# Performance work log

Measured on AMD Instinct MI355X. Metric: run time of the kernel, lower is better.

The kernel has to match this reference:

```python
import jax, jax.numpy as jnp
import numpy as np

GH, GW = 16, 16          # group_size
DIM = 512
H = 8                    # num_heads
PD = DIM // 16           # pos_dim = (dim//4)//4 = 32
B = 256                  # number of groups (batch*windows)
N = GH * GW


def _make_bias_tables():
    # biases buffer: all 2D relative offsets, shape [(2GH-1)*(2GW-1), 2]
    h = np.arange(1 - GH, GH)
    w = np.arange(1 - GW, GW)
    bh, bw = np.meshgrid(h, w, indexing='ij')
    biases = np.stack([bh, bw]).reshape(2, -1).T.astype(np.float32)
    # relative_position_index: [N, N] lookup into the bias table
    ch, cw = np.meshgrid(np.arange(GH), np.arange(GW), indexing='ij')
    coords = np.stack([ch, cw]).reshape(2, -1)            # [2, N]
    rel = coords[:, :, None] - coords[:, None, :]         # [2, N, N]
    rel = rel.transpose(1, 2, 0).copy()                   # [N, N, 2]
    rel[:, :, 0] += GH - 1
    rel[:, :, 1] += GW - 1
    rel[:, :, 0] *= 2 * GW - 1
    idx = rel.sum(-1)
    return biases, idx.astype(np.int32)


def _ln(x, g, b, eps=1e-5):
    m = x.mean(-1, keepdims=True)
    v = ((x - m) ** 2).mean(-1, keepdims=True)
    return (x - m) / jnp.sqrt(v + eps) * g + b


def setup_inputs() -> dict:
    key = jax.random.key(0)
    ks = jax.random.split(key, 16)
    s = 0.02
    biases_np, idx_np = _make_bias_tables()
    return {
        'x': jax.random.normal(ks[0], (B, N, DIM), dtype=jnp.float32),
        'qkv_w': jax.random.normal(ks[1], (DIM, 3 * DIM), dtype=jnp.float32) * s,
        'qkv_b': jnp.zeros((3 * DIM,), jnp.float32),
        'proj_w': jax.random.normal(ks[2], (DIM, DIM), dtype=jnp.float32) * s,
        'proj_b': jnp.zeros((DIM,), jnp.float32),
        'p1_w': jax.random.normal(ks[3], (2, PD), dtype=jnp.float32) * s,
        'p1_b': jnp.zeros((PD,), jnp.float32),
        'g1': jnp.ones((PD,), jnp.float32), 'b1': jnp.zeros((PD,), jnp.float32),
        'p2_w': jax.random.normal(ks[4], (PD, PD), dtype=jnp.float32) * s,
        'p2_b': jnp.zeros((PD,), jnp.float32),
        'g2': jnp.ones((PD,), jnp.float32), 'b2': jnp.zeros((PD,), jnp.float32),
        'p3_w': jax.random.normal(ks[5], (PD, PD), dtype=jnp.float32) * s,
        'p3_b': jnp.zeros((PD,), jnp.float32),
        'g3': jnp.ones((PD,), jnp.float32), 'b3': jnp.zeros((PD,), jnp.float32),
        'p4_w': jax.random.normal(ks[6], (PD, H), dtype=jnp.float32) * s,
        'p4_b': jnp.zeros((H,), jnp.float32),
        'biases': jnp.asarray(biases_np),
        'rel_idx': jnp.asarray(idx_np),
    }


def reference(x, qkv_w, qkv_b, proj_w, proj_b,
              p1_w, p1_b, g1, b1, p2_w, p2_b, g2, b2,
              p3_w, p3_b, g3, b3, p4_w, p4_b, biases, rel_idx):
    Bn, Nn, C = x.shape
    hd = C // H
    scale = hd ** -0.5
    qkv = (x @ qkv_w + qkv_b).reshape(Bn, Nn, 3, H, hd).transpose(2, 0, 3, 1, 4)
    q, k, v = qkv[0] * scale, qkv[1], qkv[2]      # [B, H, N, hd]
    attn = jnp.einsum('bhnd,bhmd->bhnm', q, k)    # [B, H, N, N]
    # dynamic position bias MLP on the offset table
    h1 = jax.nn.relu(_ln(biases @ p1_w + p1_b, g1, b1))
    h2 = jax.nn.relu(_ln(h1 @ p2_w + p2_b, g2, b2))
    h3 = jax.nn.relu(_ln(h2 @ p3_w + p3_b, g3, b3))
    pos = h3 @ p4_w + p4_b                        # [L, H]
    rpb = pos[rel_idx.reshape(-1)].reshape(Nn, Nn, H).transpose(2, 0, 1)  # [H, N, N]
    attn = jax.nn.softmax(attn + rpb[None], axis=-1)
    out = jnp.einsum('bhnm,bhmd->bhnd', attn, v)
    out = out.transpose(0, 2, 1, 3).reshape(Bn, Nn, C)
    return out @ proj_w + proj_b
```

## Files before the change

kernel.cpp:

```cpp
#include <hip/hip_runtime.h>
#include <stdint.h>

typedef __bf16 bf16x8 __attribute__((ext_vector_type(8)));
typedef float  f32x4  __attribute__((ext_vector_type(4)));
typedef unsigned short ushort_t;

#define MFMA16(a,b,c) __builtin_amdgcn_mfma_f32_16x16x32_bf16((a),(b),(c),0,0,0)

#define GLOAD16(gsrc, ldst) \
    __builtin_amdgcn_global_load_lds((const __attribute__((address_space(1))) void*)(gsrc), \
                                     (__attribute__((address_space(3))) void*)(ldst), 16, 0, 0)

#define BATCH 256
#define NTOK  256
#define DIM   512
#define NH    8
#define HD    64
#define PD    32
#define LTAB  961
#define LOG2E 1.4426950408889634f

#define POS_OFF   0
#define RPB_OFF   32768
#define WQKV_OFF  (RPB_OFF + 2097152)
#define WPROJ_OFF (WQKV_OFF + 1572864)
#define QKV_OFF   (WPROJ_OFF + 524288)
#define AOUT_OFF  (QKV_OFF + 201326592)
#define XB_OFF    AOUT_OFF

__device__ __forceinline__ ushort_t f2bf(float f) {
    unsigned int u = __builtin_bit_cast(unsigned int, f);
    u += 0x7FFFu + ((u >> 16) & 1u);
    return (ushort_t)(u >> 16);
}
__device__ __forceinline__ ushort_t cvt_bf16(float f) {
    __bf16 h = (__bf16)f;
    return __builtin_bit_cast(ushort_t, h);
}
__device__ __forceinline__ float exp2_raw(float x) {
    float r;
    asm("v_exp_f32 %0, %1" : "=v"(r) : "v"(x));
    return r;
}

#define PRO_CONV  16384
#define PRO_TQKV  (PRO_CONV + 192)
#define PRO_TPROJ (PRO_TQKV + 64)
#define PRO_TOTAL (PRO_TPROJ + 121)

__device__ __forceinline__ void transpose_body(
    const float* __restrict__ src, ushort_t* __restrict__ dst,
    int K, int Nn, int bid, int t, ushort_t (*tile)[65])
{
    int tiles_n = Nn >> 6;
    int tn = bid % tiles_n, tk = bid / tiles_n;
    int n0 = tn * 64, k0 = tk * 64;
#pragma unroll
    for (int i = 0; i < 16; i++) {
        int idx = t + i * 256;
        int kl = idx >> 6, nl = idx & 63;
        tile[nl][kl] = f2bf(src[(size_t)(k0 + kl) * Nn + n0 + nl]);
    }
    __syncthreads();
#pragma unroll
    for (int i = 0; i < 16; i++) {
        int idx = t + i * 256;
        int nl = idx >> 6, kl = idx & 63;
        dst[(size_t)(n0 + nl) * K + k0 + kl] = tile[nl][kl];
    }
}

__device__ __forceinline__ float ln_relu_t(float h, int j,
                                           const float* __restrict__ g,
                                           const float* __restrict__ bb) {
    float m = h;
    m += __shfl_xor(m, 1); m += __shfl_xor(m, 2); m += __shfl_xor(m, 4);
    m += __shfl_xor(m, 8); m += __shfl_xor(m, 16);
    m *= (1.0f / PD);
    float d = h - m;
    float v = d * d;
    v += __shfl_xor(v, 1); v += __shfl_xor(v, 2); v += __shfl_xor(v, 4);
    v += __shfl_xor(v, 8); v += __shfl_xor(v, 16);
    v *= (1.0f / PD);
    float x = d * rsqrtf(v + 1e-5f) * g[j] + bb[j];
    return x > 0.f ? x : 0.f;
}

__global__ __launch_bounds__(256) void prologue(
    const float* __restrict__ x, ushort_t* __restrict__ xb,
    const float* __restrict__ qkv_w, ushort_t* __restrict__ wqkvT,
    const float* __restrict__ proj_w, ushort_t* __restrict__ wprojT,
    const float* __restrict__ biases,
    const float* __restrict__ p1_w, const float* __restrict__ p1_b,
    const float* __restrict__ g1, const float* __restrict__ b1,
    const float* __restrict__ p2_w, const float* __restrict__ p2_b,
    const float* __restrict__ g2, const float* __restrict__ b2,
    const float* __restrict__ p3_w, const float* __restrict__ p3_b,
    const float* __restrict__ g3, const float* __restrict__ b3,
    const float* __restrict__ p4_w, const float* __restrict__ p4_b,
    float* __restrict__ pos)
{
    __shared__ ushort_t tile[64][65];
    __shared__ float hs[8][33];
    int b = blockIdx.x, tid = threadIdx.x;
    if (b < PRO_CONV) {
        size_t i = ((size_t)b * 256 + tid) * 8;
        float4 f0 = *(const float4*)(x + i);
        float4 f1 = *(const float4*)(x + i + 4);
        uint4 o;
        o.x = (unsigned)f2bf(f0.x) | ((unsigned)f2bf(f0.y) << 16);
        o.y = (unsigned)f2bf(f0.z) | ((unsigned)f2bf(f0.w) << 16);
        o.z = (unsigned)f2bf(f1.x) | ((unsigned)f2bf(f1.y) << 16);
        o.w = (unsigned)f2bf(f1.z) | ((unsigned)f2bf(f1.w) << 16);
        *reinterpret_cast<uint4*>(xb + i) = o;
    } else if (b < PRO_TQKV) {
        transpose_body(qkv_w, wqkvT, 512, 1536, b - PRO_CONV, tid, tile);
    } else if (b < PRO_TPROJ) {
        transpose_body(proj_w, wprojT, 512, 512, b - PRO_TQKV, tid, tile);
    } else {
        int rl = tid >> 5, j = tid & 31;
        int r = (b - PRO_TPROJ) * 8 + rl;
        bool ok = r < LTAB;
        float c0 = ok ? biases[r * 2 + 0] : 0.f;
        float c1 = ok ? biases[r * 2 + 1] : 0.f;

        float h = c0 * p1_w[j] + c1 * p1_w[PD + j] + p1_b[j];
        h = ln_relu_t(h, j, g1, b1);

        hs[rl][j] = h;
        __syncthreads();
        float s = p2_b[j];
#pragma unroll
        for (int i = 0; i < PD; i++) s += hs[rl][i] * p2_w[i * PD + j];
        __syncthreads();
        h = ln_relu_t(s, j, g2, b2);

        hs[rl][j] = h;
        __syncthreads();
        s = p3_b[j];
#pragma unroll
        for (int i = 0; i < PD; i++) s += hs[rl][i] * p3_w[i * PD + j];
        __syncthreads();
        h = ln_relu_t(s, j, g3, b3);

        hs[rl][j] = h;
        __syncthreads();
        if (ok && j < NH) {
            float o = p4_b[j];
#pragma unroll
            for (int i = 0; i < PD; i++) o += hs[rl][i] * p4_w[i * NH + j];
            pos[r * NH + j] = o;
        }
    }
}

#define QKV_GRID  1536
#define RPB_GRID  128
__global__ __launch_bounds__(512, 1) void qkv_gemm(
    const ushort_t* __restrict__ xb, const ushort_t* __restrict__ wT,
    const float* __restrict__ qkv_b, ushort_t* __restrict__ qkvb,
    const float* __restrict__ pos, const int* __restrict__ rel_idx,
    float* __restrict__ rpb)
{
    __shared__ ushort_t As[2][256 * 64];
    __shared__ ushort_t Bs[2][256 * 64];
    int t = threadIdx.x;
    int bid = blockIdx.x;
    if (bid >= QKV_GRID) {
        int i = (bid - QKV_GRID) * 512 + t;
        int idx = rel_idx[i];
#pragma unroll
        for (int hh = 0; hh < NH; hh++)
            rpb[(size_t)hh * 65536 + i] = pos[idx * NH + hh] * LOG2E;
        return;
    }
    int wgid = (bid & 7) * 192 + (bid >> 3);
    int mt = wgid / 6, nt = wgid % 6;
    int m0 = mt * 256, n0 = nt * 256;
    int lane = t & 63, w = t >> 6;
    int wm = w >> 2, wn = w & 3;
    int lr = lane & 15, lk = lane >> 4;
    int srow8 = lane >> 3;
    int sch = ((lane & 7) ^ srow8) * 8;
    const ushort_t* Asrc = xb + (size_t)(m0 + srow8) * 512 + sch;
    const ushort_t* Bsrc = wT + (size_t)(n0 + srow8) * 512 + sch;
    int arw = w & 3;
    int ch0 = ((lk) ^ (lr & 7)) * 8;
    int ch1 = ((4 + lk) ^ (lr & 7)) * 8;
    int arow = wm * 128 + lr;
    int brow = wn * 64 + lr;

    f32x4 acc[8][4];
#pragma unroll
    for (int fr = 0; fr < 8; fr++)
#pragma unroll
        for (int fc = 0; fc < 4; fc++) acc[fr][fc] = (f32x4){0.f, 0.f, 0.f, 0.f};

#define QSTAGE(buf, kt) do { \
    if (w < 4) { \
        _Pragma("unroll") \
        for (int i_ = 0; i_ < 8; i_++) { \
            int rb_ = arw * 64 + i_ * 8; \
            GLOAD16(Asrc + (size_t)rb_ * 512 + (kt) * 64, &As[buf][rb_ * 64]); \
        } \
    } else { \
        _Pragma("unroll") \
        for (int i_ = 0; i_ < 8; i_++) { \
            int rb_ = arw * 64 + i_ * 8; \
            GLOAD16(Bsrc + (size_t)rb_ * 512 + (kt) * 64, &Bs[buf][rb_ * 64]); \
        } \
    } } while (0)

    QSTAGE(0, 0);
    asm volatile("s_waitcnt vmcnt(0)" ::: "memory");
    __builtin_amdgcn_s_barrier();
    for (int kt = 0; kt < 8; ++kt) {
        int cb = kt & 1;
        if (kt < 7) QSTAGE(cb ^ 1, kt + 1);
        if (kt > 0) {
            if (kt < 7) asm volatile("s_waitcnt vmcnt(8)" ::: "memory");
            else        asm volatile("s_waitcnt vmcnt(0)" ::: "memory");
            __builtin_amdgcn_sched_barrier(0);
            __builtin_amdgcn_s_barrier();
        }
#pragma unroll
        for (int kh = 0; kh < 2; kh++) {
            int ch = kh ? ch1 : ch0;
            bf16x8 a[8], b[4];
#pragma unroll
            for (int fr = 0; fr < 8; fr++)
                a[fr] = *reinterpret_cast<const bf16x8*>(&As[cb][(arow + fr * 16) * 64 + ch]);
#pragma unroll
            for (int fc = 0; fc < 4; fc++)
                b[fc] = *reinterpret_cast<const bf16x8*>(&Bs[cb][(brow + fc * 16) * 64 + ch]);
#pragma unroll
            for (int fr = 0; fr < 8; fr++)
#pragma unroll
                for (int fc = 0; fc < 4; fc++)
                    acc[fr][fc] = MFMA16(a[fr], b[fc], acc[fr][fc]);
        }
        if (kt < 7) {
            __builtin_amdgcn_s_barrier();
        }
    }
#undef QSTAGE

    int s = n0 >> 9;
    int bg = m0 >> 8;
    if (s < 2) {
        float sc = (s == 0) ? 0.125f * LOG2E : 1.0f;
#pragma unroll
        for (int fc = 0; fc < 4; fc++) {
            int n = n0 + wn * 64 + fc * 16 + lr;
            float bias = qkv_b[n];
            int hh = (n >> 6) & 7, d = n & 63;
            ushort_t* dst = qkvb + ((((size_t)s * 256 + bg) * 8 + hh) * 256) * 64 + d;
#pragma unroll
            for (int fr = 0; fr < 8; fr++)
#pragma unroll
                for (int r = 0; r < 4; r++) {
                    int tok = wm * 128 + fr * 16 + lk * 4 + r;
                    dst[(size_t)tok * 64] = f2bf((acc[fr][fc][r] + bias) * sc);
                }
        }
    } else {
#pragma unroll
        for (int fc = 0; fc < 4; fc++) {
            int n = n0 + wn * 64 + fc * 16 + lr;
            float bias = qkv_b[n];
            int hh = (n >> 6) & 7, d = n & 63;
            ushort_t* dst = qkvb + ((((size_t)512 + bg) * 8 + hh) * 64 + d) * 256;
#pragma unroll
            for (int fr = 0; fr < 8; fr++) {
                int tok = wm * 128 + fr * 16 + lk * 4;
                uint2 pk;
                pk.x = (unsigned)f2bf(acc[fr][fc][0] + bias) |
                       ((unsigned)f2bf(acc[fr][fc][1] + bias) << 16);
                pk.y = (unsigned)f2bf(acc[fr][fc][2] + bias) |
                       ((unsigned)f2bf(acc[fr][fc][3] + bias) << 16);
                *reinterpret_cast<uint2*>(dst + tok) = pk;
            }
        }
    }
}

__global__ __launch_bounds__(256) void attn_kernel(
    const ushort_t* __restrict__ qkvb, const float* __restrict__ rpb,
    ushort_t* __restrict__ aout)
{
    __shared__ ushort_t Ps[4][32][40];
    __shared__ ushort_t Os[4][16 * 72];
    int t = threadIdx.x, lane = t & 63, w = t >> 6;
    int bid = blockIdx.x;
    int qh = bid & 1; int bh = bid >> 1; int hh = bh & 7; int bg = bh >> 3;
    const ushort_t* Qg  = qkvb + (((size_t)bg * 8 + hh) * 256) * 64;
    const ushort_t* Kg  = qkvb + (((size_t)(256 + bg) * 8 + hh) * 256) * 64;
    const ushort_t* VTg = qkvb + (((size_t)(512 + bg) * 8 + hh) * 64) * 256;
    int lr = lane & 15, lk = lane >> 4;
    int qrow0 = qh * 128 + w * 32;

    bf16x8 qf[2][2];
#pragma unroll
    for (int fr = 0; fr < 2; fr++)
#pragma unroll
        for (int kc = 0; kc < 2; kc++)
            qf[fr][kc] = *reinterpret_cast<const bf16x8*>(
                Qg + (size_t)(qrow0 + fr * 16 + lr) * 64 + kc * 32 + lk * 8);

    f32x4 oacc[2][4];
    float rsum[2][4];
#pragma unroll
    for (int fr = 0; fr < 2; fr++) {
#pragma unroll
        for (int fc = 0; fc < 4; fc++) oacc[fr][fc] = (f32x4){0.f, 0.f, 0.f, 0.f};
#pragma unroll
        for (int r = 0; r < 4; r++) rsum[fr][r] = 0.f;
    }

    for (int kt = 0; kt < 8; ++kt) {
        f32x4 sacc[2][2];
#pragma unroll
        for (int fr = 0; fr < 2; fr++)
#pragma unroll
            for (int fc = 0; fc < 2; fc++) sacc[fr][fc] = (f32x4){0.f, 0.f, 0.f, 0.f};
#pragma unroll
        for (int kc = 0; kc < 2; kc++) {
            bf16x8 kb0 = *reinterpret_cast<const bf16x8*>(
                Kg + (size_t)(kt * 32 + lr) * 64 + kc * 32 + lk * 8);
            bf16x8 kb1 = *reinterpret_cast<const bf16x8*>(
                Kg + (size_t)(kt * 32 + 16 + lr) * 64 + kc * 32 + lk * 8);
            sacc[0][0] = MFMA16(qf[0][kc], kb0, sacc[0][0]);
            sacc[0][1] = MFMA16(qf[0][kc], kb1, sacc[0][1]);
            sacc[1][0] = MFMA16(qf[1][kc], kb0, sacc[1][0]);
            sacc[1][1] = MFMA16(qf[1][kc], kb1, sacc[1][1]);
        }
#pragma unroll
        for (int fr = 0; fr < 2; fr++)
#pragma unroll
            for (int fc = 0; fc < 2; fc++)
#pragma unroll
                for (int r = 0; r < 4; r++) {
                    int row = qrow0 + fr * 16 + lk * 4 + r;
                    int col = kt * 32 + fc * 16 + lr;
                    float lg = sacc[fr][fc][r] + rpb[((size_t)hh * 256 + row) * 256 + col];
                    float p = exp2_raw(lg);
                    rsum[fr][r] += p;
                    Ps[w][fr * 16 + lk * 4 + r][fc * 16 + lr] = cvt_bf16(p);
                }
        bf16x8 pa[2], vb[4];
#pragma unroll
        for (int fr = 0; fr < 2; fr++)
            pa[fr] = *reinterpret_cast<const bf16x8*>(&Ps[w][fr * 16 + lr][lk * 8]);
#pragma unroll
        for (int fc = 0; fc < 4; fc++)
            vb[fc] = *reinterpret_cast<const bf16x8*>(
                VTg + (size_t)(fc * 16 + lr) * 256 + kt * 32 + lk * 8);
#pragma unroll
        for (int fr = 0; fr < 2; fr++)
#pragma unroll
            for (int fc = 0; fc < 4; fc++)
                oacc[fr][fc] = MFMA16(pa[fr], vb[fc], oacc[fr][fc]);
    }
    float rinv[2][4];
#pragma unroll
    for (int fr = 0; fr < 2; fr++)
#pragma unroll
        for (int r = 0; r < 4; r++) {
            float s = rsum[fr][r];
            s += __shfl_xor(s, 1); s += __shfl_xor(s, 2);
            s += __shfl_xor(s, 4); s += __shfl_xor(s, 8);
            rinv[fr][r] = __frcp_rn(s);
        }
#pragma unroll
    for (int fr = 0; fr < 2; fr++) {
#pragma unroll
        for (int fc = 0; fc < 4; fc++)
#pragma unroll
            for (int r = 0; r < 4; r++)
                Os[w][(lk * 4 + r) * 72 + fc * 16 + lr] = cvt_bf16(oacc[fr][fc][r] * rinv[fr][r]);
#pragma unroll
        for (int ii = 0; ii < 2; ii++) {
            int j = lane + ii * 64;
            int row = j >> 3, ch = j & 7;
            uint4 v = *reinterpret_cast<const uint4*>(&Os[w][row * 72 + ch * 8]);
            *reinterpret_cast<uint4*>(
                aout + ((size_t)(bg * 256 + qrow0 + fr * 16 + row)) * 512 + hh * 64 + ch * 8) = v;
        }
    }
}

__global__ __launch_bounds__(512, 1) void proj_gemm(
    const ushort_t* __restrict__ ain, const ushort_t* __restrict__ wT,
    const float* __restrict__ proj_b, float* __restrict__ out)
{
    __shared__ ushort_t As[2][256 * 64];
    __shared__ ushort_t Bs[2][256 * 64];
    int t = threadIdx.x;
    int bid = blockIdx.x;
    int wgid = (bid & 7) * 64 + (bid >> 3);
    int mt = wgid / 2, nt = wgid % 2;
    int m0 = mt * 256, n0 = nt * 256;
    int lane = t & 63, w = t >> 6;
    int wm = w >> 2, wn = w & 3;
    int lr = lane & 15, lk = lane >> 4;
    int srow8 = lane >> 3;
    int sch = ((lane & 7) ^ srow8) * 8;
    const ushort_t* Asrc = ain + (size_t)(m0 + srow8) * 512 + sch;
    const ushort_t* Bsrc = wT + (size_t)(n0 + srow8) * 512 + sch;
    int arw = w & 3;
    int ch0 = ((lk) ^ (lr & 7)) * 8;
    int ch1 = ((4 + lk) ^ (lr & 7)) * 8;
    int arow = wm * 128 + lr;
    int brow = wn * 64 + lr;

    f32x4 acc[8][4];
#pragma unroll
    for (int fr = 0; fr < 8; fr++)
#pragma unroll
        for (int fc = 0; fc < 4; fc++) acc[fr][fc] = (f32x4){0.f, 0.f, 0.f, 0.f};

#define PSTAGE(buf, kt) do { \
    if (w < 4) { \
        _Pragma("unroll") \
        for (int i_ = 0; i_ < 8; i_++) { \
            int rb_ = arw * 64 + i_ * 8; \
            GLOAD16(Asrc + (size_t)rb_ * 512 + (kt) * 64, &As[buf][rb_ * 64]); \
        } \
    } else { \
        _Pragma("unroll") \
        for (int i_ = 0; i_ < 8; i_++) { \
            int rb_ = arw * 64 + i_ * 8; \
            GLOAD16(Bsrc + (size_t)rb_ * 512 + (kt) * 64, &Bs[buf][rb_ * 64]); \
        } \
    } } while (0)

    PSTAGE(0, 0);
    asm volatile("s_waitcnt vmcnt(0)" ::: "memory");
    __builtin_amdgcn_s_barrier();
    for (int kt = 0; kt < 8; ++kt) {
        int cb = kt & 1;
        if (kt < 7) PSTAGE(cb ^ 1, kt + 1);
        if (kt > 0) {
            if (kt < 7) asm volatile("s_waitcnt vmcnt(8)" ::: "memory");
            else        asm volatile("s_waitcnt vmcnt(0)" ::: "memory");
            __builtin_amdgcn_sched_barrier(0);
            __builtin_amdgcn_s_barrier();
        }
#pragma unroll
        for (int kh = 0; kh < 2; kh++) {
            int ch = kh ? ch1 : ch0;
            bf16x8 a[8], b[4];
#pragma unroll
            for (int fr = 0; fr < 8; fr++)
                a[fr] = *reinterpret_cast<const bf16x8*>(&As[cb][(arow + fr * 16) * 64 + ch]);
#pragma unroll
            for (int fc = 0; fc < 4; fc++)
                b[fc] = *reinterpret_cast<const bf16x8*>(&Bs[cb][(brow + fc * 16) * 64 + ch]);
#pragma unroll
            for (int fr = 0; fr < 8; fr++)
#pragma unroll
                for (int fc = 0; fc < 4; fc++)
                    acc[fr][fc] = MFMA16(a[fr], b[fc], acc[fr][fc]);
        }
        if (kt < 7) {
            __builtin_amdgcn_s_barrier();
        }
    }
#undef PSTAGE
#pragma unroll
    for (int fc = 0; fc < 4; fc++) {
        int n = n0 + wn * 64 + fc * 16 + lr;
        float bias = proj_b[n];
#pragma unroll
        for (int fr = 0; fr < 8; fr++)
#pragma unroll
            for (int r = 0; r < 4; r++) {
                int m = m0 + wm * 128 + fr * 16 + lk * 4 + r;
                out[(size_t)m * 512 + n] = acc[fr][fc][r] + bias;
            }
    }
}

extern "C" void kernel_launch(void* const* d_in, const int* in_sizes, int n_in,
                              void* d_out, int out_size, void* d_ws, size_t ws_size,
                              hipStream_t stream) {
    const float* x      = (const float*)d_in[0];
    const float* qkv_w  = (const float*)d_in[1];
    const float* qkv_b  = (const float*)d_in[2];
    const float* proj_w = (const float*)d_in[3];
    const float* proj_b = (const float*)d_in[4];
    const float* p1_w = (const float*)d_in[5];
    const float* p1_b = (const float*)d_in[6];
    const float* g1   = (const float*)d_in[7];
    const float* b1   = (const float*)d_in[8];
    const float* p2_w = (const float*)d_in[9];
    const float* p2_b = (const float*)d_in[10];
    const float* g2   = (const float*)d_in[11];
    const float* b2   = (const float*)d_in[12];
    const float* p3_w = (const float*)d_in[13];
    const float* p3_b = (const float*)d_in[14];
    const float* g3   = (const float*)d_in[15];
    const float* b3   = (const float*)d_in[16];
    const float* p4_w = (const float*)d_in[17];
    const float* p4_b = (const float*)d_in[18];
    const float* biases  = (const float*)d_in[19];
    const int*   rel_idx = (const int*)d_in[20];
    float* out = (float*)d_out;

    char* ws = (char*)d_ws;
    float*    pos    = (float*)(ws + POS_OFF);
    float*    rpb    = (float*)(ws + RPB_OFF);
    ushort_t* wqkvT  = (ushort_t*)(ws + WQKV_OFF);
    ushort_t* wprojT = (ushort_t*)(ws + WPROJ_OFF);
    ushort_t* qkvb   = (ushort_t*)(ws + QKV_OFF);
    ushort_t* aoutb  = (ushort_t*)(ws + AOUT_OFF);
    ushort_t* xb     = (ushort_t*)(ws + XB_OFF);

    prologue<<<dim3(PRO_TOTAL), dim3(256), 0, stream>>>(
        x, xb, qkv_w, wqkvT, proj_w, wprojT, biases,
        p1_w, p1_b, g1, b1, p2_w, p2_b, g2, b2,
        p3_w, p3_b, g3, b3, p4_w, p4_b, pos);
    qkv_gemm<<<dim3(QKV_GRID + RPB_GRID), dim3(512), 0, stream>>>(
        xb, wqkvT, qkv_b, qkvb, pos, rel_idx, rpb);
    attn_kernel<<<dim3(4096), dim3(256), 0, stream>>>(qkvb, rpb, aoutb);
    proj_gemm<<<dim3(512), dim3(512), 0, stream>>>(aoutb, wprojT, proj_b, out);
}
```

Before: 369.2 us.

## Single-buffer GEMM LDS tiles to fit two workgroups per CU

After: 402.9 us. +9.1%, slower.

```diff
diff --git a/kernel.cpp b/kernel.cpp
--- a/kernel.cpp
+++ b/kernel.cpp
@@ -156,14 +156,14 @@
 
 #define QKV_GRID  1536
 #define RPB_GRID  128
-__global__ __launch_bounds__(512, 1) void qkv_gemm(
+__global__ __launch_bounds__(512, 2) void qkv_gemm(
     const ushort_t* __restrict__ xb, const ushort_t* __restrict__ wT,
     const float* __restrict__ qkv_b, ushort_t* __restrict__ qkvb,
     const float* __restrict__ pos, const int* __restrict__ rel_idx,
     float* __restrict__ rpb)
 {
-    __shared__ ushort_t As[2][256 * 64];
-    __shared__ ushort_t Bs[2][256 * 64];
+    __shared__ ushort_t As[256 * 64];
+    __shared__ ushort_t Bs[256 * 64];
     int t = threadIdx.x;
     int bid = blockIdx.x;
     if (bid >= QKV_GRID) {
@@ -196,52 +196,43 @@
 #pragma unroll
         for (int fc = 0; fc < 4; fc++) acc[fr][fc] = (f32x4){0.f, 0.f, 0.f, 0.f};
 
-#define QSTAGE(buf, kt) do { \
+#define QSTAGE(kt) do { \
     if (w < 4) { \
         _Pragma("unroll") \
         for (int i_ = 0; i_ < 8; i_++) { \
             int rb_ = arw * 64 + i_ * 8; \
-            GLOAD16(Asrc + (size_t)rb_ * 512 + (kt) * 64, &As[buf][rb_ * 64]); \
+            GLOAD16(Asrc + (size_t)rb_ * 512 + (kt) * 64, &As[rb_ * 64]); \
         } \
     } else { \
         _Pragma("unroll") \
         for (int i_ = 0; i_ < 8; i_++) { \
             int rb_ = arw * 64 + i_ * 8; \
-            GLOAD16(Bsrc + (size_t)rb_ * 512 + (kt) * 64, &Bs[buf][rb_ * 64]); \
+            GLOAD16(Bsrc + (size_t)rb_ * 512 + (kt) * 64, &Bs[rb_ * 64]); \
         } \
     } } while (0)
 
-    QSTAGE(0, 0);
-    asm volatile("s_waitcnt vmcnt(0)" ::: "memory");
-    __builtin_amdgcn_s_barrier();
     for (int kt = 0; kt < 8; ++kt) {
-        int cb = kt & 1;
-        if (kt < 7) QSTAGE(cb ^ 1, kt + 1);
-        if (kt > 0) {
-            if (kt < 7) asm volatile("s_waitcnt vmcnt(8)" ::: "memory");
-            else        asm volatile("s_waitcnt vmcnt(0)" ::: "memory");
-            __builtin_amdgcn_sched_barrier(0);
-            __builtin_amdgcn_s_barrier();
-        }
+        QSTAGE(kt);
+        asm volatile("s_waitcnt vmcnt(0)" ::: "memory");
+        __builtin_amdgcn_s_barrier();
 #pragma unroll
         for (int kh = 0; kh < 2; kh++) {
             int ch = kh ? ch1 : ch0;
             bf16x8 a[8], b[4];
 #pragma unroll
             for (int fr = 0; fr < 8; fr++)
-                a[fr] = *reinterpret_cast<const bf16x8*>(&As[cb][(arow + fr * 16) * 64 + ch]);
+                a[fr] = *reinterpret_cast<const bf16x8*>(&As[(arow + fr * 16) * 64 + ch]);
 #pragma unroll
             for (int fc = 0; fc < 4; fc++)
-                b[fc] = *reinterpret_cast<const bf16x8*>(&Bs[cb][(brow + fc * 16) * 64 + ch]);
+                b[fc] = *reinterpret_cast<const bf16x8*>(&Bs[(brow + fc * 16) * 64 + ch]);
 #pragma unroll
             for (int fr = 0; fr < 8; fr++)
 #pragma unroll
                 for (int fc = 0; fc < 4; fc++)
                     acc[fr][fc] = MFMA16(a[fr], b[fc], acc[fr][fc]);
         }
-        if (kt < 7) {
+        if (kt < 7)
             __builtin_amdgcn_s_barrier();
-        }
     }
 #undef QSTAGE
 
@@ -389,12 +380,12 @@
     }
 }
 
-__global__ __launch_bounds__(512, 1) void proj_gemm(
+__global__ __launch_bounds__(512, 2) void proj_gemm(
     const ushort_t* __restrict__ ain, const ushort_t* __restrict__ wT,
     const float* __restrict__ proj_b, float* __restrict__ out)
 {
-    __shared__ ushort_t As[2][256 * 64];
-    __shared__ ushort_t Bs[2][256 * 64];
+    __shared__ ushort_t As[256 * 64];
+    __shared__ ushort_t Bs[256 * 64];
     int t = threadIdx.x;
     int bid = blockIdx.x;
     int wgid = (bid & 7) * 64 + (bid >> 3);
@@ -419,52 +410,43 @@
 #pragma unroll
         for (int fc = 0; fc < 4; fc++) acc[fr][fc] = (f32x4){0.f, 0.f, 0.f, 0.f};
 
-#define PSTAGE(buf, kt) do { \
+#define PSTAGE(kt) do { \
     if (w < 4) { \
         _Pragma("unroll") \
         for (int i_ = 0; i_ < 8; i_++) { \
             int rb_ = arw * 64 + i_ * 8; \
-            GLOAD16(Asrc + (size_t)rb_ * 512 + (kt) * 64, &As[buf][rb_ * 64]); \
+            GLOAD16(Asrc + (size_t)rb_ * 512 + (kt) * 64, &As[rb_ * 64]); \
         } \
     } else { \
         _Pragma("unroll") \
         for (int i_ = 0; i_ < 8; i_++) { \
             int rb_ = arw * 64 + i_ * 8; \
-            GLOAD16(Bsrc + (size_t)rb_ * 512 + (kt) * 64, &Bs[buf][rb_ * 64]); \
+            GLOAD16(Bsrc + (size_t)rb_ * 512 + (kt) * 64, &Bs[rb_ * 64]); \
         } \
     } } while (0)
 
-    PSTAGE(0, 0);
-    asm volatile("s_waitcnt vmcnt(0)" ::: "memory");
-    __builtin_amdgcn_s_barrier();
     for (int kt = 0; kt < 8; ++kt) {
-        int cb = kt & 1;
-        if (kt < 7) PSTAGE(cb ^ 1, kt + 1);
-        if (kt > 0) {
-            if (kt < 7) asm volatile("s_waitcnt vmcnt(8)" ::: "memory");
-            else        asm volatile("s_waitcnt vmcnt(0)" ::: "memory");
-            __builtin_amdgcn_sched_barrier(0);
-            __builtin_amdgcn_s_barrier();
-        }
+        PSTAGE(kt);
+        asm volatile("s_waitcnt vmcnt(0)" ::: "memory");
+        __builtin_amdgcn_s_barrier();
 #pragma unroll
         for (int kh = 0; kh < 2; kh++) {
             int ch = kh ? ch1 : ch0;
             bf16x8 a[8], b[4];
 #pragma unroll
             for (int fr = 0; fr < 8; fr++)
-                a[fr] = *reinterpret_cast<const bf16x8*>(&As[cb][(arow + fr * 16) * 64 + ch]);
+                a[fr] = *reinterpret_cast<const bf16x8*>(&As[(arow + fr * 16) * 64 + ch]);
 #pragma unroll
             for (int fc = 0; fc < 4; fc++)
-                b[fc] = *reinterpret_cast<const bf16x8*>(&Bs[cb][(brow + fc * 16) * 64 + ch]);
+                b[fc] = *reinterpret_cast<const bf16x8*>(&Bs[(brow + fc * 16) * 64 + ch]);
 #pragma unroll
             for (int fr = 0; fr < 8; fr++)
 #pragma unroll
                 for (int fc = 0; fc < 4; fc++)
                     acc[fr][fc] = MFMA16(a[fr], b[fc], acc[fr][fc]);
         }
-        if (kt < 7) {
+        if (kt < 7)
             __builtin_amdgcn_s_barrier();
-        }
     }
 #undef PSTAGE
 #pragma unroll
```
